# Optimization experiments

Measured on AMD Instinct MI355X. Metric: run time of the kernel, lower is better.

## Reference

```python
import jax, jax.numpy as jnp
import numpy as np
from jax import lax

RADIUS = 3
ITERATION = 6
KSIZE = 2 * RADIUS + 1


def _make_kernels(r):
    # Build the 8 directional side-window box kernels, order: L,R,U,D,NW,NE,SW,SE
    k = 2 * r + 1
    f = np.ones((k, k), np.float32)
    L = f.copy(); L[:, r + 1:] = 0
    R = f.copy(); R[:, :r] = 0
    U = f.copy(); U[r + 1:, :] = 0
    D = f.copy(); D[:r, :] = 0
    NW = U.copy(); NW[:, r + 1:] = 0
    NE = U.copy(); NE[:, :r] = 0
    SW = D.copy(); SW[:, r + 1:] = 0
    SE = D.copy(); SE[:, :r] = 0
    n_half = (r + 1) * k          # normalizer for half windows
    n_quarter = (r + 1) ** 2      # normalizer for quarter windows
    ks = np.stack([L / n_half, R / n_half, U / n_half, D / n_half,
                   NW / n_quarter, NE / n_quarter, SW / n_quarter, SE / n_quarter])
    return jnp.asarray(ks[:, None, :, :])  # (8,1,k,k) OIHW


def setup_inputs() -> dict:
    key = jax.random.key(0)
    k1, k2 = jax.random.split(key)
    im = jax.random.normal(k1, (4, 3, 512, 512), dtype=jnp.float32)
    pert = jax.random.normal(k2, (4, 3, 512, 512), dtype=jnp.float32)
    return {"im": im, "pert": pert}


def reference(im, pert):
    b, c, h, w = im.shape
    W = _make_kernels(RADIUS)

    def conv8(x):  # (N,1,h,w) -> (N,8,h,w), SAME padding of radius
        return lax.conv_general_dilated(
            x, W, window_strides=(1, 1),
            padding=[(RADIUS, RADIUS), (RADIUS, RADIUS)],
            dimension_numbers=("NCHW", "OIHW", "NCHW"))

    # channels are processed independently with identical kernels -> fold c into batch
    im_f = im.reshape(b * c, 1, h, w)
    pert_f = pert.reshape(b * c, 1, h, w)

    def step(carry, _):
        im_ch, pert_ch = carry
        z = jnp.concatenate([im_ch, pert_ch], axis=0)  # (2N,1,h,w)
        dz = conv8(z) - z                              # (2N,8,h,w), broadcast over dir
        d, dd = jnp.split(dz, 2, axis=0)
        idx = jnp.argmin(jnp.abs(d), axis=1, keepdims=True)    # (N,1,h,w)
        dm = jnp.take_along_axis(d, idx, axis=1)
        ddm = jnp.take_along_axis(dd, idx, axis=1)
        return (im_ch + dm, pert_ch + ddm), None

    (im_f, pert_f), _ = lax.scan(step, (im_f, pert_f), None, length=ITERATION)
    # torch code overwrites every channel of res with pert_ch -> result is filtered pert
    return pert_f.reshape(b, c, h, w)
```

## Files before the change

kernel.cpp:

```cpp
#include <hip/hip_runtime.h>

#define HH 512
#define WW 512
#define NIMG 12
#define RAD 3
#define TW 64
#define TH 16
#define LW (TW + 2*RAD)
#define LH (TH + 2*RAD)
#define RPW 4

__global__ __launch_bounds__(256) void swf_step(
    const float* __restrict__ im_in, const float* __restrict__ pe_in,
    float* __restrict__ im_out, float* __restrict__ pe_out)
{
    __shared__ float sI[LH][LW];
    __shared__ float sP[LH][LW];

    const int tid = threadIdx.x;
    const int x0 = blockIdx.x * TW;
    const int y0 = blockIdx.y * TH;
    const size_t base = (size_t)blockIdx.z * (size_t)(HH * WW);
    const float* imb = im_in + base;
    const float* peb = pe_in + base;

    for (int i = tid; i < LH * LW; i += 256) {
        int r = i / LW;
        int c = i - r * LW;
        int gy = y0 - RAD + r;
        int gx = x0 - RAD + c;
        bool ok = ((unsigned)gy < (unsigned)HH) && ((unsigned)gx < (unsigned)WW);
        int gi = gy * WW + gx;
        sI[r][c] = ok ? imb[gi] : 0.0f;
        sP[r][c] = ok ? peb[gi] : 0.0f;
    }
    __syncthreads();

    const float w28 = 1.0f / 28.0f;
    const float w16 = 0.0625f;
    const int tx = tid & 63;
    const int wv = tid >> 6;
    const int r0 = wv * RPW;

    float wi[7][7];
    float hl[7], hr[7], cc[7];

    #pragma unroll
    for (int m = 0; m < 7; ++m) {
        #pragma unroll
        for (int dx = 0; dx < 7; ++dx)
            wi[m][dx] = sI[r0 + m][tx + dx];
        float b0 = sP[r0 + m][tx],     b1 = sP[r0 + m][tx + 1],
              b2 = sP[r0 + m][tx + 2], b3 = sP[r0 + m][tx + 3],
              b4 = sP[r0 + m][tx + 4], b5 = sP[r0 + m][tx + 5],
              b6 = sP[r0 + m][tx + 6];
        hl[m] = (b0 + b1) + (b2 + b3);
        hr[m] = (b3 + b4) + (b5 + b6);
        cc[m] = b3;
    }

    #pragma unroll
    for (int jj = 0; jj < RPW; ++jj) {
        float d[8];
        {
            float sL = 0.f, sR = 0.f, sU = 0.f, sD = 0.f;
            float sNW = 0.f, sNE = 0.f, sSW = 0.f, sSE = 0.f;
            #pragma unroll
            for (int dy = 0; dy < 7; ++dy) {
                const int s = (jj + dy) % 7;
                #pragma unroll
                for (int dx = 0; dx < 4; ++dx)
                    sL = fmaf(wi[s][dx], w28, sL);
                #pragma unroll
                for (int dx = 3; dx < 7; ++dx)
                    sR = fmaf(wi[s][dx], w28, sR);
            }
            #pragma unroll
            for (int dy = 0; dy < 4; ++dy) {
                const int s = (jj + dy) % 7;
                #pragma unroll
                for (int dx = 0; dx < 7; ++dx)
                    sU = fmaf(wi[s][dx], w28, sU);
                #pragma unroll
                for (int dx = 0; dx < 4; ++dx)
                    sNW = fmaf(wi[s][dx], w16, sNW);
                #pragma unroll
                for (int dx = 3; dx < 7; ++dx)
                    sNE = fmaf(wi[s][dx], w16, sNE);
            }
            #pragma unroll
            for (int dy = 3; dy < 7; ++dy) {
                const int s = (jj + dy) % 7;
                #pragma unroll
                for (int dx = 0; dx < 7; ++dx)
                    sD = fmaf(wi[s][dx], w28, sD);
                #pragma unroll
                for (int dx = 0; dx < 4; ++dx)
                    sSW = fmaf(wi[s][dx], w16, sSW);
                #pragma unroll
                for (int dx = 3; dx < 7; ++dx)
                    sSE = fmaf(wi[s][dx], w16, sSE);
            }
            const float cI = wi[(jj + 3) % 7][3];
            d[0] = sL - cI;  d[1] = sR - cI;  d[2] = sU - cI;  d[3] = sD - cI;
            d[4] = sNW - cI; d[5] = sNE - cI; d[6] = sSW - cI; d[7] = sSE - cI;
        }

        float e[8];
        const int p0 = (jj + 0) % 7, p1 = (jj + 1) % 7, p2 = (jj + 2) % 7,
                  p3 = (jj + 3) % 7, p4 = (jj + 4) % 7, p5 = (jj + 5) % 7,
                  p6 = (jj + 6) % 7;
        {
            float qnw = ((hl[p0] + hl[p1]) + (hl[p2] + hl[p3]));
            float qsw = ((hl[p3] + hl[p4]) + (hl[p5] + hl[p6]));
            float qne = ((hr[p0] + hr[p1]) + (hr[p2] + hr[p3]));
            float qse = ((hr[p3] + hr[p4]) + (hr[p5] + hr[p6]));
            float cu  = ((cc[p0] + cc[p1]) + (cc[p2] + cc[p3]));
            float cd  = ((cc[p3] + cc[p4]) + (cc[p5] + cc[p6]));
            float cP  = cc[p3];
            e[0] = (qnw + qsw - hl[p3]) * w28 - cP;
            e[1] = (qne + qse - hr[p3]) * w28 - cP;
            e[2] = (qnw + qne - cu)     * w28 - cP;
            e[3] = (qsw + qse - cd)     * w28 - cP;
            e[4] = qnw * w16 - cP;
            e[5] = qne * w16 - cP;
            e[6] = qsw * w16 - cP;
            e[7] = qse * w16 - cP;
        }

        float bestAbs = fabsf(d[0]);
        float bd = d[0];
        float be = e[0];
        #pragma unroll
        for (int j = 1; j < 8; ++j) {
            float a = fabsf(d[j]);
            bool take = a < bestAbs;
            bestAbs = take ? a : bestAbs;
            bd = take ? d[j] : bd;
            be = take ? e[j] : be;
        }

        const int gy = y0 + r0 + jj;
        const int gx = x0 + tx;
        const size_t gi = base + (size_t)gy * WW + gx;
        im_out[gi] = wi[(jj + 3) % 7][3] + bd;
        pe_out[gi] = cc[p3] + be;

        if (jj < RPW - 1) {
            const int m = r0 + jj + 7;
            const int slot = jj % 7;
            #pragma unroll
            for (int dx = 0; dx < 7; ++dx)
                wi[slot][dx] = sI[m][tx + dx];
            float b0 = sP[m][tx],     b1 = sP[m][tx + 1], b2 = sP[m][tx + 2],
                  b3 = sP[m][tx + 3], b4 = sP[m][tx + 4], b5 = sP[m][tx + 5],
                  b6 = sP[m][tx + 6];
            hl[slot] = (b0 + b1) + (b2 + b3);
            hr[slot] = (b3 + b4) + (b5 + b6);
            cc[slot] = b3;
        }
    }
}

extern "C" void kernel_launch(void* const* d_in, const int* in_sizes, int n_in,
                              void* d_out, int out_size, void* d_ws, size_t ws_size,
                              hipStream_t stream) {
    const float* im0 = (const float*)d_in[0];
    const float* pe0 = (const float*)d_in[1];
    float* out = (float*)d_out;

    const size_t npix = (size_t)NIMG * HH * WW;
    float* imA = (float*)d_ws;
    float* imB = imA + npix;
    float* peA = imB + npix;
    float* peB = out;

    dim3 grid(WW / TW, HH / TH, NIMG);
    dim3 block(256);

    swf_step<<<grid, block, 0, stream>>>(im0, pe0, imA, peA);
    swf_step<<<grid, block, 0, stream>>>(imA, peA, imB, peB);
    swf_step<<<grid, block, 0, stream>>>(imB, peB, imA, peA);
    swf_step<<<grid, block, 0, stream>>>(imA, peA, imB, peB);
    swf_step<<<grid, block, 0, stream>>>(imB, peB, imA, peA);
    swf_step<<<grid, block, 0, stream>>>(imA, peA, imB, out);
}
```

Measured before the change: 241.6 us.

## Fuse pairs of filter iterations per launch with halo recomputation in shared memory

Each launch now loads a tile with a doubled halo and computes one full iteration over the extended region into shared memory, then a second iteration from that intermediate. This halves the number of launches and the global memory round trips. The last launch skips storing the image plane because only the perturbation result is returned. The cost is redundant halo computation, a scalar per-pixel loop for the first pass that reloads 49-element windows from LDS, and a larger LDS footprint that may reduce occupancy.

After: 314.2 us. +30.1%, slower.

```diff
diff --git a/kernel.cpp b/kernel.cpp
--- a/kernel.cpp
+++ b/kernel.cpp
@@ -6,16 +6,107 @@
 #define RAD 3
 #define TW 64
 #define TH 16
-#define LW (TW + 2*RAD)
-#define LH (TH + 2*RAD)
 #define RPW 4
-
-__global__ __launch_bounds__(256) void swf_step(
+#define SIH (TH + 4*RAD)
+#define SIW (TW + 4*RAD)
+#define SMH (TH + 2*RAD)
+#define SMW (TW + 2*RAD)
+
+
+__device__ __forceinline__ void swf_px(
+    const float w[7][7],
+    float hl[7], float hr[7],
+    float cc[7],
+    float& outI, float& outP)
+{
+    const float w28 = 1.0f / 28.0f;
+    const float w16 = 0.0625f;
+
+    float d[8];
+    {
+        float sL = 0.f, sR = 0.f, sU = 0.f, sD = 0.f;
+        float sNW = 0.f, sNE = 0.f, sSW = 0.f, sSE = 0.f;
+        #pragma unroll
+        for (int dy = 0; dy < 7; ++dy) {
+            #pragma unroll
+            for (int dx = 0; dx < 4; ++dx)
+                sL = fmaf(w[dy][dx], w28, sL);
+            #pragma unroll
+            for (int dx = 3; dx < 7; ++dx)
+                sR = fmaf(w[dy][dx], w28, sR);
+        }
+        #pragma unroll
+        for (int dy = 0; dy < 4; ++dy) {
+            #pragma unroll
+            for (int dx = 0; dx < 7; ++dx)
+                sU = fmaf(w[dy][dx], w28, sU);
+            #pragma unroll
+            for (int dx = 0; dx < 4; ++dx)
+                sNW = fmaf(w[dy][dx], w16, sNW);
+            #pragma unroll
+            for (int dx = 3; dx < 7; ++dx)
+                sNE = fmaf(w[dy][dx], w16, sNE);
+        }
+        #pragma unroll
+        for (int dy = 3; dy < 7; ++dy) {
+            #pragma unroll
+            for (int dx = 0; dx < 7; ++dx)
+                sD = fmaf(w[dy][dx], w28, sD);
+            #pragma unroll
+            for (int dx = 0; dx < 4; ++dx)
+                sSW = fmaf(w[dy][dx], w16, sSW);
+            #pragma unroll
+            for (int dx = 3; dx < 7; ++dx)
+                sSE = fmaf(w[dy][dx], w16, sSE);
+        }
+        const float cI = w[3][3];
+        d[0] = sL - cI;  d[1] = sR - cI;  d[2] = sU - cI;  d[3] = sD - cI;
+        d[4] = sNW - cI; d[5] = sNE - cI; d[6] = sSW - cI; d[7] = sSE - cI;
+        outI = cI;
+    }
+
+    float e[8];
+    {
+        float qnw = ((hl[0] + hl[1]) + (hl[2] + hl[3]));
+        float qsw = ((hl[3] + hl[4]) + (hl[5] + hl[6]));
+        float qne = ((hr[0] + hr[1]) + (hr[2] + hr[3]));
+        float qse = ((hr[3] + hr[4]) + (hr[5] + hr[6]));
+        float cu  = ((cc[0] + cc[1]) + (cc[2] + cc[3]));
+        float cd  = ((cc[3] + cc[4]) + (cc[5] + cc[6]));
+        float cP  = cc[3];
+        e[0] = (qnw + qsw - hl[3]) * w28 - cP;
+        e[1] = (qne + qse - hr[3]) * w28 - cP;
+        e[2] = (qnw + qne - cu)    * w28 - cP;
+        e[3] = (qsw + qse - cd)    * w28 - cP;
+        e[4] = qnw * w16 - cP;
+        e[5] = qne * w16 - cP;
+        e[6] = qsw * w16 - cP;
+        e[7] = qse * w16 - cP;
+        outP = cP;
+    }
+
+    float bestAbs = fabsf(d[0]);
+    float bd = d[0];
+    float be = e[0];
+    #pragma unroll
+    for (int j = 1; j < 8; ++j) {
+        float a = fabsf(d[j]);
+        bool take = a < bestAbs;
+        bestAbs = take ? a : bestAbs;
+        bd = take ? d[j] : bd;
+        be = take ? e[j] : be;
+    }
+    outI += bd;
+    outP += be;
+}
+
+template <bool STORE_IM>
+__global__ __launch_bounds__(256) void swf_fused(
     const float* __restrict__ im_in, const float* __restrict__ pe_in,
     float* __restrict__ im_out, float* __restrict__ pe_out)
 {
-    __shared__ float sI[LH][LW];
-    __shared__ float sP[LH][LW];
+    __shared__ float sIn[2][SIH][SIW];
+    __shared__ float sMd[2][SMH][SMW];
 
     const int tid = threadIdx.x;
     const int x0 = blockIdx.x * TW;
@@ -24,36 +115,63 @@
     const float* imb = im_in + base;
     const float* peb = pe_in + base;
 
-    for (int i = tid; i < LH * LW; i += 256) {
-        int r = i / LW;
-        int c = i - r * LW;
-        int gy = y0 - RAD + r;
-        int gx = x0 - RAD + c;
+    for (int i = tid; i < SIH * SIW; i += 256) {
+        int r = i / SIW;
+        int c = i - r * SIW;
+        int gy = y0 - 2 * RAD + r;
+        int gx = x0 - 2 * RAD + c;
         bool ok = ((unsigned)gy < (unsigned)HH) && ((unsigned)gx < (unsigned)WW);
         int gi = gy * WW + gx;
-        sI[r][c] = ok ? imb[gi] : 0.0f;
-        sP[r][c] = ok ? peb[gi] : 0.0f;
+        sIn[0][r][c] = ok ? imb[gi] : 0.0f;
+        sIn[1][r][c] = ok ? peb[gi] : 0.0f;
     }
     __syncthreads();
 
-    const float w28 = 1.0f / 28.0f;
-    const float w16 = 0.0625f;
+    for (int i = tid; i < SMH * SMW; i += 256) {
+        int r = i / SMW;
+        int c = i - r * SMW;
+        int iy = y0 - RAD + r;
+        int ix = x0 - RAD + c;
+        bool inside = ((unsigned)iy < (unsigned)HH) && ((unsigned)ix < (unsigned)WW);
+        float oI = 0.0f, oP = 0.0f;
+        if (inside) {
+            float w[7][7];
+            float hl[7], hr[7], cc[7];
+            #pragma unroll
+            for (int dy = 0; dy < 7; ++dy) {
+                #pragma unroll
+                for (int dx = 0; dx < 7; ++dx)
+                    w[dy][dx] = sIn[0][r + dy][c + dx];
+                float b0 = sIn[1][r + dy][c],     b1 = sIn[1][r + dy][c + 1],
+                      b2 = sIn[1][r + dy][c + 2], b3 = sIn[1][r + dy][c + 3],
+                      b4 = sIn[1][r + dy][c + 4], b5 = sIn[1][r + dy][c + 5],
+                      b6 = sIn[1][r + dy][c + 6];
+                hl[dy] = (b0 + b1) + (b2 + b3);
+                hr[dy] = (b3 + b4) + (b5 + b6);
+                cc[dy] = b3;
+            }
+            swf_px(w, hl, hr, cc, oI, oP);
+        }
+        sMd[0][r][c] = oI;
+        sMd[1][r][c] = oP;
+    }
+    __syncthreads();
+
     const int tx = tid & 63;
     const int wv = tid >> 6;
     const int r0 = wv * RPW;
 
     float wi[7][7];
     float hl[7], hr[7], cc[7];
-
     #pragma unroll
     for (int m = 0; m < 7; ++m) {
         #pragma unroll
         for (int dx = 0; dx < 7; ++dx)
-            wi[m][dx] = sI[r0 + m][tx + dx];
-        float b0 = sP[r0 + m][tx],     b1 = sP[r0 + m][tx + 1],
-              b2 = sP[r0 + m][tx + 2], b3 = sP[r0 + m][tx + 3],
-              b4 = sP[r0 + m][tx + 4], b5 = sP[r0 + m][tx + 5],
-              b6 = sP[r0 + m][tx + 6];
+            wi[m][dx] = sMd[0][r0 + m][tx + dx];
+        float b0 = sMd[1][r0 + m][tx],     b1 = sMd[1][r0 + m][tx + 1],
+              b2 = sMd[1][r0 + m][tx + 2], b3 = sMd[1][r0 + m][tx + 3],
+              b4 = sMd[1][r0 + m][tx + 4], b5 = sMd[1][r0 + m][tx + 5],
+              b6 = sMd[1][r0 + m][tx + 6];
         hl[m] = (b0 + b1) + (b2 + b3);
         hr[m] = (b3 + b4) + (b5 + b6);
         cc[m] = b3;
@@ -61,100 +179,37 @@
 
     #pragma unroll
     for (int jj = 0; jj < RPW; ++jj) {
-        float d[8];
-        {
-            float sL = 0.f, sR = 0.f, sU = 0.f, sD = 0.f;
-            float sNW = 0.f, sNE = 0.f, sSW = 0.f, sSE = 0.f;
-            #pragma unroll
-            for (int dy = 0; dy < 7; ++dy) {
-                const int s = (jj + dy) % 7;
-                #pragma unroll
-                for (int dx = 0; dx < 4; ++dx)
-                    sL = fmaf(wi[s][dx], w28, sL);
-                #pragma unroll
-                for (int dx = 3; dx < 7; ++dx)
-                    sR = fmaf(wi[s][dx], w28, sR);
-            }
-            #pragma unroll
-            for (int dy = 0; dy < 4; ++dy) {
-                const int s = (jj + dy) % 7;
-                #pragma unroll
-                for (int dx = 0; dx < 7; ++dx)
-                    sU = fmaf(wi[s][dx], w28, sU);
-                #pragma unroll
-                for (int dx = 0; dx < 4; ++dx)
-                    sNW = fmaf(wi[s][dx], w16, sNW);
-                #pragma unroll
-                for (int dx = 3; dx < 7; ++dx)
-                    sNE = fmaf(wi[s][dx], w16, sNE);
-            }
-            #pragma unroll
-            for (int dy = 3; dy < 7; ++dy) {
-                const int s = (jj + dy) % 7;
-                #pragma unroll
-                for (int dx = 0; dx < 7; ++dx)
-                    sD = fmaf(wi[s][dx], w28, sD);
-                #pragma unroll
-                for (int dx = 0; dx < 4; ++dx)
-                    sSW = fmaf(wi[s][dx], w16, sSW);
-                #pragma unroll
-                for (int dx = 3; dx < 7; ++dx)
-                    sSE = fmaf(wi[s][dx], w16, sSE);
-            }
-            const float cI = wi[(jj + 3) % 7][3];
-            d[0] = sL - cI;  d[1] = sR - cI;  d[2] = sU - cI;  d[3] = sD - cI;
-            d[4] = sNW - cI; d[5] = sNE - cI; d[6] = sSW - cI; d[7] = sSE - cI;
-        }
-
-        float e[8];
-        const int p0 = (jj + 0) % 7, p1 = (jj + 1) % 7, p2 = (jj + 2) % 7,
-                  p3 = (jj + 3) % 7, p4 = (jj + 4) % 7, p5 = (jj + 5) % 7,
-                  p6 = (jj + 6) % 7;
-        {
-            float qnw = ((hl[p0] + hl[p1]) + (hl[p2] + hl[p3]));
-            float qsw = ((hl[p3] + hl[p4]) + (hl[p5] + hl[p6]));
-            float qne = ((hr[p0] + hr[p1]) + (hr[p2] + hr[p3]));
-            float qse = ((hr[p3] + hr[p4]) + (hr[p5] + hr[p6]));
-            float cu  = ((cc[p0] + cc[p1]) + (cc[p2] + cc[p3]));
-            float cd  = ((cc[p3] + cc[p4]) + (cc[p5] + cc[p6]));
-            float cP  = cc[p3];
-            e[0] = (qnw + qsw - hl[p3]) * w28 - cP;
-            e[1] = (qne + qse - hr[p3]) * w28 - cP;
-            e[2] = (qnw + qne - cu)     * w28 - cP;
-            e[3] = (qsw + qse - cd)     * w28 - cP;
-            e[4] = qnw * w16 - cP;
-            e[5] = qne * w16 - cP;
-            e[6] = qsw * w16 - cP;
-            e[7] = qse * w16 - cP;
-        }
-
-        float bestAbs = fabsf(d[0]);
-        float bd = d[0];
-        float be = e[0];
-        #pragma unroll
-        for (int j = 1; j < 8; ++j) {
-            float a = fabsf(d[j]);
-            bool take = a < bestAbs;
-            bestAbs = take ? a : bestAbs;
-            bd = take ? d[j] : bd;
-            be = take ? e[j] : be;
-        }
+        float w[7][7];
+        float hl2[7], hr2[7], cc2[7];
+        #pragma unroll
+        for (int dy = 0; dy < 7; ++dy) {
+            const int s = (jj + dy) % 7;
+            #pragma unroll
+            for (int dx = 0; dx < 7; ++dx)
+                w[dy][dx] = wi[s][dx];
+            hl2[dy] = hl[s];
+            hr2[dy] = hr[s];
+            cc2[dy] = cc[s];
+        }
+        float oI, oP;
+        swf_px(w, hl2, hr2, cc2, oI, oP);
 
         const int gy = y0 + r0 + jj;
         const int gx = x0 + tx;
         const size_t gi = base + (size_t)gy * WW + gx;
-        im_out[gi] = wi[(jj + 3) % 7][3] + bd;
-        pe_out[gi] = cc[p3] + be;
+        if (STORE_IM) im_out[gi] = oI;
+        pe_out[gi] = oP;
 
         if (jj < RPW - 1) {
             const int m = r0 + jj + 7;
             const int slot = jj % 7;
             #pragma unroll
             for (int dx = 0; dx < 7; ++dx)
-                wi[slot][dx] = sI[m][tx + dx];
-            float b0 = sP[m][tx],     b1 = sP[m][tx + 1], b2 = sP[m][tx + 2],
-                  b3 = sP[m][tx + 3], b4 = sP[m][tx + 4], b5 = sP[m][tx + 5],
-                  b6 = sP[m][tx + 6];
+                wi[slot][dx] = sMd[0][m][tx + dx];
+            float b0 = sMd[1][m][tx],     b1 = sMd[1][m][tx + 1],
+                  b2 = sMd[1][m][tx + 2], b3 = sMd[1][m][tx + 3],
+                  b4 = sMd[1][m][tx + 4], b5 = sMd[1][m][tx + 5],
+                  b6 = sMd[1][m][tx + 6];
             hl[slot] = (b0 + b1) + (b2 + b3);
             hr[slot] = (b3 + b4) + (b5 + b6);
             cc[slot] = b3;
@@ -173,15 +228,12 @@
     float* imA = (float*)d_ws;
     float* imB = imA + npix;
     float* peA = imB + npix;
-    float* peB = out;
+    float* peB = peA + npix;
 
     dim3 grid(WW / TW, HH / TH, NIMG);
     dim3 block(256);
 
-    swf_step<<<grid, block, 0, stream>>>(im0, pe0, imA, peA);
-    swf_step<<<grid, block, 0, stream>>>(imA, peA, imB, peB);
-    swf_step<<<grid, block, 0, stream>>>(imB, peB, imA, peA);
-    swf_step<<<grid, block, 0, stream>>>(imA, peA, imB, peB);
-    swf_step<<<grid, block, 0, stream>>>(imB, peB, imA, peA);
-    swf_step<<<grid, block, 0, stream>>>(imA, peA, imB, out);
+    swf_fused<true ><<<grid, block, 0, stream>>>(im0, pe0, imA, peA);
+    swf_fused<true ><<<grid, block, 0, stream>>>(imA, peA, imB, peB);
+    swf_fused<false><<<grid, block, 0, stream>>>(imB, peB, imA, out);
 }
```

## Fuse two filter iterations per kernel using halo recompute in shared memory

Applied to the files above, without the earlier changes.

Each kernel now loads a tile with a doubled halo and computes one iteration over the tile plus a one-radius halo into a second shared buffer. It then runs the second iteration from that buffer, which cuts the launch count from six to three and halves global round trips of the intermediate images. The last launch skips storing the image array, since only the filtered pert is returned. In exchange, each block does redundant halo work in a scalar per-element loop and uses more shared memory. That may reduce occupancy and adds cost on the recompute pass.

Measured after the change: 312.4 us. +29.3%, slower.

```diff
diff --git a/kernel.cpp b/kernel.cpp
--- a/kernel.cpp
+++ b/kernel.cpp
@@ -6,16 +6,23 @@
 #define RAD 3
 #define TW 64
 #define TH 16
-#define LW (TW + 2*RAD)
-#define LH (TH + 2*RAD)
 #define RPW 4
-
-__global__ __launch_bounds__(256) void swf_step(
+#define SIH (TH + 4*RAD)
+#define SIW (TW + 4*RAD)
+#define SIP (SIW + 1)
+#define SMH (TH + 2*RAD)
+#define SMW (TW + 2*RAD)
+#define SMP (SMW + 1)
+
+template <bool STORE_IM>
+__global__ __launch_bounds__(256) void swf_fused(
     const float* __restrict__ im_in, const float* __restrict__ pe_in,
     float* __restrict__ im_out, float* __restrict__ pe_out)
 {
-    __shared__ float sI[LH][LW];
-    __shared__ float sP[LH][LW];
+    __shared__ float sI0[SIH][SIP];
+    __shared__ float sP0[SIH][SIP];
+    __shared__ float sIm[SMH][SMP];
+    __shared__ float sPm[SMH][SMP];
 
     const int tid = threadIdx.x;
     const int x0 = blockIdx.x * TW;
@@ -24,36 +31,128 @@
     const float* imb = im_in + base;
     const float* peb = pe_in + base;
 
-    for (int i = tid; i < LH * LW; i += 256) {
-        int r = i / LW;
-        int c = i - r * LW;
-        int gy = y0 - RAD + r;
-        int gx = x0 - RAD + c;
+    const float w28 = 1.0f / 28.0f;
+    const float w16 = 0.0625f;
+
+    for (int i = tid; i < SIH * SIW; i += 256) {
+        int r = i / SIW;
+        int c = i - r * SIW;
+        int gy = y0 - 2 * RAD + r;
+        int gx = x0 - 2 * RAD + c;
         bool ok = ((unsigned)gy < (unsigned)HH) && ((unsigned)gx < (unsigned)WW);
         int gi = gy * WW + gx;
-        sI[r][c] = ok ? imb[gi] : 0.0f;
-        sP[r][c] = ok ? peb[gi] : 0.0f;
+        sI0[r][c] = ok ? imb[gi] : 0.0f;
+        sP0[r][c] = ok ? peb[gi] : 0.0f;
     }
     __syncthreads();
 
-    const float w28 = 1.0f / 28.0f;
-    const float w16 = 0.0625f;
+    for (int i = tid; i < SMH * SMW; i += 256) {
+        int r = i / SMW;
+        int c = i - r * SMW;
+        int iy = y0 - RAD + r;
+        int ix = x0 - RAD + c;
+        bool inside = ((unsigned)iy < (unsigned)HH) && ((unsigned)ix < (unsigned)WW);
+        float oI = 0.0f, oP = 0.0f;
+        if (inside) {
+            float sL = 0.f, sR = 0.f, sU = 0.f, sD = 0.f;
+            float sNW = 0.f, sNE = 0.f, sSW = 0.f, sSE = 0.f;
+            float hl[7], hr[7], cb[7];
+            #pragma unroll
+            for (int dy = 0; dy < 7; ++dy) {
+                float a0 = sI0[r + dy][c],     a1 = sI0[r + dy][c + 1],
+                      a2 = sI0[r + dy][c + 2], a3 = sI0[r + dy][c + 3],
+                      a4 = sI0[r + dy][c + 4], a5 = sI0[r + dy][c + 5],
+                      a6 = sI0[r + dy][c + 6];
+                sL = fmaf(a0, w28, sL); sL = fmaf(a1, w28, sL);
+                sL = fmaf(a2, w28, sL); sL = fmaf(a3, w28, sL);
+                sR = fmaf(a3, w28, sR); sR = fmaf(a4, w28, sR);
+                sR = fmaf(a5, w28, sR); sR = fmaf(a6, w28, sR);
+                if (dy < 4) {
+                    sU = fmaf(a0, w28, sU); sU = fmaf(a1, w28, sU);
+                    sU = fmaf(a2, w28, sU); sU = fmaf(a3, w28, sU);
+                    sU = fmaf(a4, w28, sU); sU = fmaf(a5, w28, sU);
+                    sU = fmaf(a6, w28, sU);
+                    sNW = fmaf(a0, w16, sNW); sNW = fmaf(a1, w16, sNW);
+                    sNW = fmaf(a2, w16, sNW); sNW = fmaf(a3, w16, sNW);
+                    sNE = fmaf(a3, w16, sNE); sNE = fmaf(a4, w16, sNE);
+                    sNE = fmaf(a5, w16, sNE); sNE = fmaf(a6, w16, sNE);
+                }
+                if (dy >= 3) {
+                    sD = fmaf(a0, w28, sD); sD = fmaf(a1, w28, sD);
+                    sD = fmaf(a2, w28, sD); sD = fmaf(a3, w28, sD);
+                    sD = fmaf(a4, w28, sD); sD = fmaf(a5, w28, sD);
+                    sD = fmaf(a6, w28, sD);
+                    sSW = fmaf(a0, w16, sSW); sSW = fmaf(a1, w16, sSW);
+                    sSW = fmaf(a2, w16, sSW); sSW = fmaf(a3, w16, sSW);
+                    sSE = fmaf(a3, w16, sSE); sSE = fmaf(a4, w16, sSE);
+                    sSE = fmaf(a5, w16, sSE); sSE = fmaf(a6, w16, sSE);
+                }
+                float b0 = sP0[r + dy][c],     b1 = sP0[r + dy][c + 1],
+                      b2 = sP0[r + dy][c + 2], b3 = sP0[r + dy][c + 3],
+                      b4 = sP0[r + dy][c + 4], b5 = sP0[r + dy][c + 5],
+                      b6 = sP0[r + dy][c + 6];
+                hl[dy] = (b0 + b1) + (b2 + b3);
+                hr[dy] = (b3 + b4) + (b5 + b6);
+                cb[dy] = b3;
+            }
+            const float cI = sI0[r + 3][c + 3];
+            float d[8];
+            d[0] = sL - cI;  d[1] = sR - cI;  d[2] = sU - cI;  d[3] = sD - cI;
+            d[4] = sNW - cI; d[5] = sNE - cI; d[6] = sSW - cI; d[7] = sSE - cI;
+
+            float e[8];
+            {
+                float qnw = ((hl[0] + hl[1]) + (hl[2] + hl[3]));
+                float qsw = ((hl[3] + hl[4]) + (hl[5] + hl[6]));
+                float qne = ((hr[0] + hr[1]) + (hr[2] + hr[3]));
+                float qse = ((hr[3] + hr[4]) + (hr[5] + hr[6]));
+                float cu  = ((cb[0] + cb[1]) + (cb[2] + cb[3]));
+                float cd  = ((cb[3] + cb[4]) + (cb[5] + cb[6]));
+                float cP  = cb[3];
+                e[0] = (qnw + qsw - hl[3]) * w28 - cP;
+                e[1] = (qne + qse - hr[3]) * w28 - cP;
+                e[2] = (qnw + qne - cu)    * w28 - cP;
+                e[3] = (qsw + qse - cd)    * w28 - cP;
+                e[4] = qnw * w16 - cP;
+                e[5] = qne * w16 - cP;
+                e[6] = qsw * w16 - cP;
+                e[7] = qse * w16 - cP;
+                oP = cP;
+            }
+            float bestAbs = fabsf(d[0]);
+            float bd = d[0];
+            float be = e[0];
+            #pragma unroll
+            for (int j = 1; j < 8; ++j) {
+                float a = fabsf(d[j]);
+                bool take = a < bestAbs;
+                bestAbs = take ? a : bestAbs;
+                bd = take ? d[j] : bd;
+                be = take ? e[j] : be;
+            }
+            oI = cI + bd;
+            oP += be;
+        }
+        sIm[r][c] = oI;
+        sPm[r][c] = oP;
+    }
+    __syncthreads();
+
     const int tx = tid & 63;
     const int wv = tid >> 6;
     const int r0 = wv * RPW;
 
     float wi[7][7];
     float hl[7], hr[7], cc[7];
-
     #pragma unroll
     for (int m = 0; m < 7; ++m) {
         #pragma unroll
         for (int dx = 0; dx < 7; ++dx)
-            wi[m][dx] = sI[r0 + m][tx + dx];
-        float b0 = sP[r0 + m][tx],     b1 = sP[r0 + m][tx + 1],
-              b2 = sP[r0 + m][tx + 2], b3 = sP[r0 + m][tx + 3],
-              b4 = sP[r0 + m][tx + 4], b5 = sP[r0 + m][tx + 5],
-              b6 = sP[r0 + m][tx + 6];
+            wi[m][dx] = sIm[r0 + m][tx + dx];
+        float b0 = sPm[r0 + m][tx],     b1 = sPm[r0 + m][tx + 1],
+              b2 = sPm[r0 + m][tx + 2], b3 = sPm[r0 + m][tx + 3],
+              b4 = sPm[r0 + m][tx + 4], b5 = sPm[r0 + m][tx + 5],
+              b6 = sPm[r0 + m][tx + 6];
         hl[m] = (b0 + b1) + (b2 + b3);
         hr[m] = (b3 + b4) + (b5 + b6);
         cc[m] = b3;
@@ -143,7 +242,7 @@
         const int gy = y0 + r0 + jj;
         const int gx = x0 + tx;
         const size_t gi = base + (size_t)gy * WW + gx;
-        im_out[gi] = wi[(jj + 3) % 7][3] + bd;
+        if (STORE_IM) im_out[gi] = wi[(jj + 3) % 7][3] + bd;
         pe_out[gi] = cc[p3] + be;
 
         if (jj < RPW - 1) {
@@ -151,10 +250,10 @@
             const int slot = jj % 7;
             #pragma unroll
             for (int dx = 0; dx < 7; ++dx)
-                wi[slot][dx] = sI[m][tx + dx];
-            float b0 = sP[m][tx],     b1 = sP[m][tx + 1], b2 = sP[m][tx + 2],
-                  b3 = sP[m][tx + 3], b4 = sP[m][tx + 4], b5 = sP[m][tx + 5],
-                  b6 = sP[m][tx + 6];
+                wi[slot][dx] = sIm[m][tx + dx];
+            float b0 = sPm[m][tx],     b1 = sPm[m][tx + 1], b2 = sPm[m][tx + 2],
+                  b3 = sPm[m][tx + 3], b4 = sPm[m][tx + 4], b5 = sPm[m][tx + 5],
+                  b6 = sPm[m][tx + 6];
             hl[slot] = (b0 + b1) + (b2 + b3);
             hr[slot] = (b3 + b4) + (b5 + b6);
             cc[slot] = b3;
@@ -173,15 +272,12 @@
     float* imA = (float*)d_ws;
     float* imB = imA + npix;
     float* peA = imB + npix;
-    float* peB = out;
+    float* peB = peA + npix;
 
     dim3 grid(WW / TW, HH / TH, NIMG);
     dim3 block(256);
 
-    swf_step<<<grid, block, 0, stream>>>(im0, pe0, imA, peA);
-    swf_step<<<grid, block, 0, stream>>>(imA, peA, imB, peB);
-    swf_step<<<grid, block, 0, stream>>>(imB, peB, imA, peA);
-    swf_step<<<grid, block, 0, stream>>>(imA, peA, imB, peB);
-    swf_step<<<grid, block, 0, stream>>>(imB, peB, imA, peA);
-    swf_step<<<grid, block, 0, stream>>>(imA, peA, imB, out);
+    swf_fused<true ><<<grid, block, 0, stream>>>(im0, pe0, imA, peA);
+    swf_fused<true ><<<grid, block, 0, stream>>>(imA, peA, imB, peB);
+    swf_fused<false><<<grid, block, 0, stream>>>(imB, peB, imA, out);
 }
```
